# Kernel tuning notes

Measured on AMD Instinct MI355X. Metric: run time of the kernel, lower is better.

Reference implementation:

```python
import jax, jax.numpy as jnp
import numpy as np
import math

B, L, D = 4, 2048, 512
H = 8
HD = D // H
K1 = 64  # local_window_size
K2 = 64  # global_window_size


def semi_local_mask(seq_len):
    # Faithful to create_semi_local_mask: anti-diagonal band + global prefix, ANDed with causal tril.
    i = jnp.arange(seq_len)[:, None]
    j = jnp.arange(seq_len)[None, :]
    band = (i + j >= seq_len - K1) & (i + j <= seq_len)
    glob = (j <= K2) & (j <= seq_len - i)
    causal = j <= i
    return (band | glob) & causal  # [L, L] bool


def setup_inputs() -> dict:
    key = jax.random.key(0)
    ks = jax.random.split(key, 8)
    def xavier(k, shape):
        fan_in, fan_out = shape[1], shape[0]
        lim = math.sqrt(6.0 / (fan_in + fan_out))
        return jax.random.uniform(k, shape, jnp.float32, -lim, lim)
    x = jax.random.normal(ks[0], (B, L, D), jnp.float32)
    w_qkv = xavier(ks[1], (3 * D, D)); b_qkv = jnp.zeros((3 * D,), jnp.float32)
    w_u = xavier(ks[2], (D, D));       b_u = jnp.zeros((D,), jnp.float32)
    w_out = xavier(ks[3], (D, D));     b_out = jnp.zeros((D,), jnp.float32)
    return {"x": x, "w_qkv": w_qkv, "b_qkv": b_qkv, "w_u": w_u, "b_u": b_u,
            "w_out": w_out, "b_out": b_out}


def reference(x, w_qkv, b_qkv, w_u, b_u, w_out, b_out):
    Bsz, Lq, Dm = x.shape
    qkv = (x @ w_qkv.T + b_qkv).reshape(Bsz, Lq, 3, H, HD)
    q, k, v = jnp.moveaxis(qkv, 2, 0)            # each [B, L, H, HD]
    q = jnp.transpose(q, (0, 2, 1, 3))           # [B, H, L, HD]
    k = jnp.transpose(k, (0, 2, 1, 3))
    v = jnp.transpose(v, (0, 2, 1, 3))
    u = x @ w_u.T + b_u                          # [B, L, D] (gate values)
    scale = 1.0 / math.sqrt(HD)
    scores = jnp.einsum('bhqd,bhkd->bhqk', q * scale, k)
    mask = semi_local_mask(Lq)                   # [L, L]
    scores = jnp.where(mask[None, None], scores, -jnp.inf)
    attn = jax.nn.softmax(scores, axis=-1)
    out = jnp.einsum('bhqk,bhkd->bhqd', attn, v)
    out = jnp.transpose(out, (0, 2, 1, 3)).reshape(Bsz, Lq, Dm)
    out = jax.nn.silu(out) * u
    return out @ w_out.T + b_out
```

## Files before the change

### kernel.cpp

```cpp
#include <hip/hip_runtime.h>
#include <hip/hip_bf16.h>

typedef __bf16 bf16x8 __attribute__((ext_vector_type(8)));
typedef float f32x4 __attribute__((ext_vector_type(4)));

#define B_ 4
#define L_ 2048
#define D_ 512
#define H_ 8

__device__ __forceinline__ void gl16(const __bf16* g, __bf16* l) {
  __builtin_amdgcn_global_load_lds(
      (const __attribute__((address_space(1))) void*)g,
      (__attribute__((address_space(3))) void*)l, 16, 0, 0);
}

__global__ __launch_bounds__(256) void cvt_pack(
    const float* __restrict__ x, const float* __restrict__ wq,
    const float* __restrict__ wu, const float* __restrict__ wo,
    const float* __restrict__ bq, const float* __restrict__ bu,
    __bf16* __restrict__ xb, __bf16* __restrict__ wcat,
    __bf16* __restrict__ wob, float* __restrict__ bcat)
{
  const int idx8 = blockIdx.x * 256 + threadIdx.x;
  const float* src; __bf16* dst; size_t so, dof;
  if (idx8 < 524288)      { src = x;  dst = xb;   so = (size_t)idx8 * 8;            dof = so; }
  else if (idx8 < 622592) { src = wq; dst = wcat; so = (size_t)(idx8 - 524288) * 8; dof = so; }
  else if (idx8 < 655360) { src = wu; dst = wcat; so = (size_t)(idx8 - 622592) * 8; dof = so + 786432; }
  else                    { src = wo; dst = wob;  so = (size_t)(idx8 - 655360) * 8; dof = so; }
  const float4 lo = *(const float4*)(src + so);
  const float4 hi = *(const float4*)(src + so + 4);
  bf16x8 r;
  r[0] = (__bf16)lo.x; r[1] = (__bf16)lo.y; r[2] = (__bf16)lo.z; r[3] = (__bf16)lo.w;
  r[4] = (__bf16)hi.x; r[5] = (__bf16)hi.y; r[6] = (__bf16)hi.z; r[7] = (__bf16)hi.w;
  *(bf16x8*)(dst + dof) = r;
  if (blockIdx.x == 0) {
#pragma unroll
    for (int e = 0; e < 8; ++e) {
      const int col = threadIdx.x * 8 + e;
      bcat[col] = (col < 1536) ? bq[col] : bu[col - 1536];
    }
  }
}

__global__ __launch_bounds__(512, 2) void gemm256(
    const __bf16* __restrict__ A, const __bf16* __restrict__ W,
    const float* __restrict__ bias, __bf16* __restrict__ C,
    int M, int N, int K)
{
  extern __shared__ char smem[];
  const int t = threadIdx.x;
  const int lane = t & 63;
  const int wave = t >> 6;
  const int wm = (wave >> 2) * 128;
  const int wn = (wave & 3) * 64;
  const int bm0 = blockIdx.x * 256;
  const int bn0 = blockIdx.y * 256;
  const int r = lane & 15, q = lane >> 4;
  const int nt = K >> 6;

  auto stage = [&](int kt, int p) {
#pragma unroll
    for (int j = 0; j < 4; ++j) {
      const int c = t + j * 512;
      const int row = c >> 3;
      const int cs = (c & 7) ^ (row & 7);
      gl16(A + (size_t)(bm0 + row) * K + kt * 64 + cs * 8,
           (__bf16*)(smem + p * 32768) + c * 8);
    }
#pragma unroll
    for (int j = 0; j < 4; ++j) {
      const int c = t + j * 512;
      const int row = c >> 3;
      const int cs = (c & 7) ^ (row & 7);
      gl16(W + (size_t)(bn0 + row) * K + kt * 64 + cs * 8,
           (__bf16*)(smem + 65536 + p * 32768) + c * 8);
    }
  };
  auto rdA = [&](int p, int mi, int ks) -> bf16x8 {
    const int row = wm + mi * 16 + r;
    const int byte = row * 128 + ((ks * 64 + q * 16) ^ ((row & 7) << 4));
    return *(const bf16x8*)(smem + p * 32768 + byte);
  };
  auto rdB = [&](int p, int ni, int ks) -> bf16x8 {
    const int row = wn + ni * 16 + r;
    const int byte = row * 128 + ((ks * 64 + q * 16) ^ ((row & 7) << 4));
    return *(const bf16x8*)(smem + 65536 + p * 32768 + byte);
  };

#define SB0 __builtin_amdgcn_sched_barrier(0)
#define LGKM0 asm volatile("s_waitcnt lgkmcnt(0)" ::: "memory")

  f32x4 acc[8][4] = {};

  stage(0, 0);
  stage(1, 1);

  for (int kt = 0; kt < nt; ++kt) {
    const int p = kt & 1;
    if (kt < nt - 1) asm volatile("s_waitcnt vmcnt(8)" ::: "memory");
    else             asm volatile("s_waitcnt vmcnt(0)" ::: "memory");
    SB0;
    __builtin_amdgcn_s_barrier();
    SB0;

    bf16x8 a03[4][2], a47[4][2], b01[2][2], b23[2][2];
#pragma unroll
    for (int mi = 0; mi < 4; ++mi) { a03[mi][0] = rdA(p, mi, 0); a03[mi][1] = rdA(p, mi, 1); }
#pragma unroll
    for (int ni = 0; ni < 2; ++ni) { b01[ni][0] = rdB(p, ni, 0); b01[ni][1] = rdB(p, ni, 1); }
    SB0; __builtin_amdgcn_s_barrier(); LGKM0; SB0;
    __builtin_amdgcn_s_setprio(1);
#pragma unroll
    for (int mi = 0; mi < 4; ++mi)
#pragma unroll
      for (int ni = 0; ni < 2; ++ni) {
        acc[mi][ni] = __builtin_amdgcn_mfma_f32_16x16x32_bf16(a03[mi][0], b01[ni][0], acc[mi][ni], 0, 0, 0);
        acc[mi][ni] = __builtin_amdgcn_mfma_f32_16x16x32_bf16(a03[mi][1], b01[ni][1], acc[mi][ni], 0, 0, 0);
      }
    __builtin_amdgcn_s_setprio(0);
    SB0; __builtin_amdgcn_s_barrier(); SB0;
#pragma unroll
    for (int ni = 0; ni < 2; ++ni) { b23[ni][0] = rdB(p, ni + 2, 0); b23[ni][1] = rdB(p, ni + 2, 1); }
    SB0; __builtin_amdgcn_s_barrier(); LGKM0; SB0;
    __builtin_amdgcn_s_setprio(1);
#pragma unroll
    for (int mi = 0; mi < 4; ++mi)
#pragma unroll
      for (int ni = 0; ni < 2; ++ni) {
        acc[mi][ni + 2] = __builtin_amdgcn_mfma_f32_16x16x32_bf16(a03[mi][0], b23[ni][0], acc[mi][ni + 2], 0, 0, 0);
        acc[mi][ni + 2] = __builtin_amdgcn_mfma_f32_16x16x32_bf16(a03[mi][1], b23[ni][1], acc[mi][ni + 2], 0, 0, 0);
      }
    __builtin_amdgcn_s_setprio(0);
    SB0; __builtin_amdgcn_s_barrier(); SB0;
#pragma unroll
    for (int mi = 0; mi < 4; ++mi) { a47[mi][0] = rdA(p, mi + 4, 0); a47[mi][1] = rdA(p, mi + 4, 1); }
    SB0; __builtin_amdgcn_s_barrier(); LGKM0; SB0;
    __builtin_amdgcn_s_setprio(1);
#pragma unroll
    for (int mi = 0; mi < 4; ++mi)
#pragma unroll
      for (int ni = 0; ni < 2; ++ni) {
        acc[mi + 4][ni] = __builtin_amdgcn_mfma_f32_16x16x32_bf16(a47[mi][0], b01[ni][0], acc[mi + 4][ni], 0, 0, 0);
        acc[mi + 4][ni] = __builtin_amdgcn_mfma_f32_16x16x32_bf16(a47[mi][1], b01[ni][1], acc[mi + 4][ni], 0, 0, 0);
      }
    __builtin_amdgcn_s_setprio(0);
    SB0; __builtin_amdgcn_s_barrier(); SB0;
    if (kt + 2 < nt) stage(kt + 2, p);
    __builtin_amdgcn_s_setprio(1);
#pragma unroll
    for (int mi = 0; mi < 4; ++mi)
#pragma unroll
      for (int ni = 0; ni < 2; ++ni) {
        acc[mi + 4][ni + 2] = __builtin_amdgcn_mfma_f32_16x16x32_bf16(a47[mi][0], b23[ni][0], acc[mi + 4][ni + 2], 0, 0, 0);
        acc[mi + 4][ni + 2] = __builtin_amdgcn_mfma_f32_16x16x32_bf16(a47[mi][1], b23[ni][1], acc[mi + 4][ni + 2], 0, 0, 0);
      }
    __builtin_amdgcn_s_setprio(0);
  }

  const int cc = lane & 15, cq = lane >> 4;
#pragma unroll
  for (int mi = 0; mi < 8; ++mi) {
#pragma unroll
    for (int ni = 0; ni < 4; ++ni) {
      const int gcol = bn0 + wn + ni * 16 + cc;
      const float bv = bias[gcol];
#pragma unroll
      for (int rr = 0; rr < 4; ++rr) {
        const int grow = bm0 + wm + mi * 16 + cq * 4 + rr;
        C[(size_t)grow * N + gcol] = (__bf16)(acc[mi][ni][rr] + bv);
      }
    }
  }
}

template <typename TOUT>
__global__ __launch_bounds__(256) void gemm_async(
    const __bf16* __restrict__ A, const __bf16* __restrict__ W,
    const float* __restrict__ bias, TOUT* __restrict__ C,
    int M, int N, int K)
{
  __shared__ __bf16 lA[4096];
  __shared__ __bf16 lB[4096];
  const int t = threadIdx.x;
  const int lane = t & 63;
  const int wave = t >> 6;
  const int bm0 = blockIdx.x * 128;
  const int bn0 = blockIdx.y * 128;
  const int wm = (wave >> 1) * 64;
  const int wn = (wave & 1) * 64;

  f32x4 acc[4][4] = {};

  const __bf16* Ap0 = A + (size_t)(bm0 + (t >> 2)) * K + (t & 3) * 8;
  const __bf16* Bp0 = W + (size_t)(bn0 + (t >> 2)) * K + (t & 3) * 8;
  const size_t r64 = (size_t)64 * K;

  for (int k0 = 0; k0 < K; k0 += 32) {
    __syncthreads();
    gl16(Ap0 + k0,       lA + t * 8);
    gl16(Ap0 + r64 + k0, lA + (t + 256) * 8);
    gl16(Bp0 + k0,       lB + t * 8);
    gl16(Bp0 + r64 + k0, lB + (t + 256) * 8);
    __syncthreads();

    const int r = lane & 15, q = lane >> 4;
    bf16x8 af[4], bfr[4];
#pragma unroll
    for (int mi = 0; mi < 4; ++mi) af[mi] = ((const bf16x8*)lA)[(wm + mi * 16 + r) * 4 + q];
#pragma unroll
    for (int ni = 0; ni < 4; ++ni) bfr[ni] = ((const bf16x8*)lB)[(wn + ni * 16 + r) * 4 + q];
#pragma unroll
    for (int mi = 0; mi < 4; ++mi)
#pragma unroll
      for (int ni = 0; ni < 4; ++ni)
        acc[mi][ni] = __builtin_amdgcn_mfma_f32_16x16x32_bf16(af[mi], bfr[ni], acc[mi][ni], 0, 0, 0);
  }

  const int cc = lane & 15, cq = lane >> 4;
#pragma unroll
  for (int mi = 0; mi < 4; ++mi) {
#pragma unroll
    for (int ni = 0; ni < 4; ++ni) {
      const int gcol = bn0 + wn + ni * 16 + cc;
      const float bv = bias[gcol];
#pragma unroll
      for (int rr = 0; rr < 4; ++rr) {
        const int grow = bm0 + wm + mi * 16 + cq * 4 + rr;
        C[(size_t)grow * N + gcol] = (TOUT)(acc[mi][ni][rr] + bv);
      }
    }
  }
}

#define SP 72
#define QS 2048
__global__ __launch_bounds__(256) void attn_tile(
    const __bf16* __restrict__ qu,
    __bf16* __restrict__ g)
{
  const int qt = blockIdx.x, h = blockIdx.y, b = blockIdx.z;
  const int t = threadIdx.x;
  const int lane = t & 63;
  const int w = t >> 6;
  const int q0 = qt * 64, qmax = q0 + 63;
  const size_t bL = (size_t)b * L_;

  __shared__ __bf16 lK[4096];
  __shared__ __bf16 lV[64 * SP];
  __shared__ __bf16 Pb[64 * SP];

  const int cq = lane >> 4, cc = lane & 15;
  const int krow_st = t >> 2, kgb = t & 3;

  bf16x8 aq0, aq1;
  {
    const __bf16* qsrc = qu + (bL + q0 + w * 16 + cc) * QS + h * 64 + cq * 8;
    aq0 = *(const bf16x8*)qsrc;
    aq1 = *(const bf16x8*)(qsrc + 32);
  }

  float mreg[4], lreg[4];
#pragma unroll
  for (int rr = 0; rr < 4; ++rr) { mreg[rr] = -1e30f; lreg[rr] = 0.f; }
  f32x4 acc_o[4] = {};

  int clist[5]; int ncl = 0;
  clist[ncl++] = 0;
  if (qmax >= 64) clist[ncl++] = 64;
  {
    int lo = 1921 - q0; if (lo < 0) lo = 0; lo &= ~63;
    const int hik = min(qmax, 2048 - q0);
    for (int c = lo; c <= hik; c += 64)
      if (c >= 128) clist[ncl++] = c;
  }

  bf16x8 k0r, k1r, var, vbr;
  {
    const __bf16* src = qu + (bL + clist[0] + krow_st) * QS + 512 + h * 64;
    k0r = *(const bf16x8*)(src + kgb * 8);
    k1r = *(const bf16x8*)(src + kgb * 8 + 32);
    const __bf16* vsrc = qu + (bL + clist[0] + lane) * QS + 1024 + h * 64 + w * 16;
    var = *(const bf16x8*)vsrc;
    vbr = *(const bf16x8*)(vsrc + 8);
  }

  for (int ci = 0; ci < ncl; ++ci) {
    const int c0 = clist[ci];
    asm volatile("s_waitcnt vmcnt(0)" ::: "memory");
    __builtin_amdgcn_sched_barrier(0);
    __builtin_amdgcn_s_barrier();
    __builtin_amdgcn_sched_barrier(0);
    {
      char* lkb = (char*)lK;
      const int sw = (krow_st & 7) << 4;
      *(bf16x8*)(lkb + ((krow_st * 128 + kgb * 16) ^ sw))      = k0r;
      *(bf16x8*)(lkb + ((krow_st * 128 + kgb * 16 + 64) ^ sw)) = k1r;
#pragma unroll
      for (int e = 0; e < 8; ++e) {
        lV[(w * 16 + e) * SP + lane]     = var[e];
        lV[(w * 16 + 8 + e) * SP + lane] = vbr[e];
      }
    }
    if (ci + 1 < ncl) {
      const int cn = clist[ci + 1];
      const __bf16* src = qu + (bL + cn + krow_st) * QS + 512 + h * 64;
      k0r = *(const bf16x8*)(src + kgb * 8);
      k1r = *(const bf16x8*)(src + kgb * 8 + 32);
      const __bf16* vsrc = qu + (bL + cn + lane) * QS + 1024 + h * 64 + w * 16;
      var = *(const bf16x8*)(vsrc);
      vbr = *(const bf16x8*)(vsrc + 8);
    }
    asm volatile("s_waitcnt lgkmcnt(0)" ::: "memory");
    __builtin_amdgcn_sched_barrier(0);
    __builtin_amdgcn_s_barrier();
    __builtin_amdgcn_sched_barrier(0);

    f32x4 s[4];
    {
      const char* lkb = (const char*)lK;
#pragma unroll
      for (int nt = 0; nt < 4; ++nt) {
        const int krow = nt * 16 + cc;
        const int sw = (krow & 7) << 4;
        bf16x8 bk0 = *(const bf16x8*)(lkb + ((krow * 128 + cq * 16) ^ sw));
        bf16x8 bk1 = *(const bf16x8*)(lkb + ((krow * 128 + 64 + cq * 16) ^ sw));
        f32x4 a = {};
        a = __builtin_amdgcn_mfma_f32_16x16x32_bf16(aq0, bk0, a, 0, 0, 0);
        a = __builtin_amdgcn_mfma_f32_16x16x32_bf16(aq1, bk1, a, 0, 0, 0);
        s[nt] = a;
      }
    }

#pragma unroll
    for (int nt = 0; nt < 4; ++nt) {
#pragma unroll
      for (int rr = 0; rr < 4; ++rr) {
        const int i = q0 + w * 16 + cq * 4 + rr;
        const int j = c0 + nt * 16 + cc;
        const int ij = i + j;
        const bool valid = (j <= i) &&
            ((ij >= 1984 && ij <= 2048) || (j <= 64 && ij <= 2048));
        s[nt][rr] = valid ? s[nt][rr] * 0.125f : -1e30f;
      }
    }

    f32x4 pm;
#pragma unroll
    for (int rr = 0; rr < 4; ++rr)
      pm[rr] = fmaxf(fmaxf(s[0][rr], s[1][rr]), fmaxf(s[2][rr], s[3][rr]));
#pragma unroll
    for (int m = 1; m < 16; m <<= 1) {
#pragma unroll
      for (int rr = 0; rr < 4; ++rr)
        pm[rr] = fmaxf(pm[rr], __shfl_xor(pm[rr], m, 64));
    }
    float corr[4];
#pragma unroll
    for (int rr = 0; rr < 4; ++rr) {
      const float nm = fmaxf(mreg[rr], pm[rr]);
      corr[rr] = __expf(mreg[rr] - nm);
      mreg[rr] = nm;
    }

    f32x4 ps = {};
#pragma unroll
    for (int nt = 0; nt < 4; ++nt) {
#pragma unroll
      for (int rr = 0; rr < 4; ++rr) {
        const float p = __expf(s[nt][rr] - mreg[rr]);
        ps[rr] += p;
        Pb[(w * 16 + cq * 4 + rr) * SP + nt * 16 + cc] = (__bf16)p;
      }
    }
#pragma unroll
    for (int m = 1; m < 16; m <<= 1) {
#pragma unroll
      for (int rr = 0; rr < 4; ++rr)
        ps[rr] += __shfl_xor(ps[rr], m, 64);
    }
#pragma unroll
    for (int rr = 0; rr < 4; ++rr) lreg[rr] = lreg[rr] * corr[rr] + ps[rr];

    {
      bf16x8 pa0 = *(const bf16x8*)(Pb + (w * 16 + cc) * SP + cq * 8);
      bf16x8 pa1 = *(const bf16x8*)(Pb + (w * 16 + cc) * SP + 32 + cq * 8);
#pragma unroll
      for (int dt = 0; dt < 4; ++dt) {
#pragma unroll
        for (int rr = 0; rr < 4; ++rr) acc_o[dt][rr] *= corr[rr];
        bf16x8 vb0 = *(const bf16x8*)(lV + (dt * 16 + cc) * SP + cq * 8);
        bf16x8 vb1 = *(const bf16x8*)(lV + (dt * 16 + cc) * SP + 32 + cq * 8);
        acc_o[dt] = __builtin_amdgcn_mfma_f32_16x16x32_bf16(pa0, vb0, acc_o[dt], 0, 0, 0);
        acc_o[dt] = __builtin_amdgcn_mfma_f32_16x16x32_bf16(pa1, vb1, acc_o[dt], 0, 0, 0);
      }
    }
  }

#pragma unroll
  for (int dt = 0; dt < 4; ++dt) {
#pragma unroll
    for (int rr = 0; rr < 4; ++rr) {
      const int row16 = cq * 4 + rr;
      const size_t qrow = bL + q0 + w * 16 + row16;
      const int d = dt * 16 + cc;
      const float o = acc_o[dt][rr] / fmaxf(lreg[rr], 1e-30f);
      const float uv = (float)qu[qrow * QS + 1536 + h * 64 + d];
      g[qrow * D_ + h * 64 + d] = (__bf16)(o / (1.f + __expf(-o)) * uv);
    }
  }
}

extern "C" void kernel_launch(void* const* d_in, const int* in_sizes, int n_in,
                              void* d_out, int out_size, void* d_ws, size_t ws_size,
                              hipStream_t stream) {
  const float* x     = (const float*)d_in[0];
  const float* w_qkv = (const float*)d_in[1];
  const float* b_qkv = (const float*)d_in[2];
  const float* w_u   = (const float*)d_in[3];
  const float* b_u   = (const float*)d_in[4];
  const float* w_out = (const float*)d_in[5];
  const float* b_out = (const float*)d_in[6];
  float* out = (float*)d_out;

  char* ws = (char*)d_ws;
  __bf16* xb   = (__bf16*)ws;
  __bf16* wcat = (__bf16*)(ws + 8388608);
  __bf16* wob  = (__bf16*)(ws + 10485760);
  float*  bcat = (float*) (ws + 11010048);
  __bf16* qu   = (__bf16*)(ws + 11018240);
  __bf16* gb   = (__bf16*)(ws + 44572672);

  static bool attr_done = []() {
    hipFuncSetAttribute((const void*)gemm256,
                        hipFuncAttributeMaxDynamicSharedMemorySize, 131072);
    return true;
  }();
  (void)attr_done;

  cvt_pack<<<dim3(2688), dim3(256), 0, stream>>>(
      x, w_qkv, w_u, w_out, b_qkv, b_u, xb, wcat, wob, bcat);
  gemm256<<<dim3(32, 8), dim3(512), 131072, stream>>>(
      xb, wcat, bcat, qu, 8192, 2048, 512);
  attn_tile<<<dim3(L_ / 64, H_, B_), dim3(256), 0, stream>>>(qu, gb);
  gemm_async<float><<<dim3(64, 4), dim3(256), 0, stream>>>(
      gb, wob, b_out, out, 8192, 512, 512);
}
```

Baseline: 148.3 us.

## Fuse all stages into one cooperative persistent kernel with grid syncs

Adds a cooperative megakernel that runs the fp32-to-bf16 conversion, the QKV/U GEMM, the semi-local attention and the output GEMM in sequence. Grid-wide syncs separate the stages, so the four separate launches and their gaps go away. The attention stage packs two 64-row tiles per 512-thread block, and the output GEMM now uses 128x128 tiles across 256 blocks. It also removes several intra-iteration LDS barriers in the standalone GEMM, which is a race risk because shared buffers may be restaged before every wave has finished reading. With 256 blocks the attention work is less parallel, and any block skew stalls the whole grid at each sync.

```diff
diff --git a/kernel.cpp b/kernel.cpp
--- a/kernel.cpp
+++ b/kernel.cpp
@@ -1,5 +1,8 @@
 #include <hip/hip_runtime.h>
 #include <hip/hip_bf16.h>
+#include <hip/hip_cooperative_groups.h>
+
+namespace cg = cooperative_groups;
 
 typedef __bf16 bf16x8 __attribute__((ext_vector_type(8)));
 typedef float f32x4 __attribute__((ext_vector_type(4)));
@@ -8,11 +11,433 @@
 #define L_ 2048
 #define D_ 512
 #define H_ 8
+#define QS 2048
+#define SP 72
+
+#define SB0 __builtin_amdgcn_sched_barrier(0)
+#define WAIT_VM(n) asm volatile("s_waitcnt vmcnt(" #n ")" ::: "memory")
+#define WAIT_LGKM0 asm volatile("s_waitcnt lgkmcnt(0)" ::: "memory")
 
 __device__ __forceinline__ void gl16(const __bf16* g, __bf16* l) {
   __builtin_amdgcn_global_load_lds(
       (const __attribute__((address_space(1))) void*)g,
       (__attribute__((address_space(3))) void*)l, 16, 0, 0);
+}
+
+__global__ __launch_bounds__(512, 2) void mega(
+    const float* __restrict__ x,  const float* __restrict__ wq,
+    const float* __restrict__ wu, const float* __restrict__ wo,
+    const float* __restrict__ bq, const float* __restrict__ bu,
+    const float* __restrict__ bo,
+    __bf16* __restrict__ xb, __bf16* __restrict__ wcat,
+    __bf16* __restrict__ wob, float* __restrict__ bcat,
+    __bf16* __restrict__ qu, __bf16* __restrict__ gb,
+    float* __restrict__ out)
+{
+  extern __shared__ char smem[];
+  cg::grid_group gg = cg::this_grid();
+  const int t = threadIdx.x;
+  const int blk = blockIdx.x;
+  const int lane = t & 63;
+  const int wave = t >> 6;
+
+  {
+#pragma unroll
+    for (int it = 0; it < 6; ++it) {
+      const int idx8 = blk * 512 + t + it * 131072;
+      if (idx8 < 688128) {
+        const float* src; __bf16* dst; size_t so, dof;
+        if (idx8 < 524288)      { src = x;  dst = xb;   so = (size_t)idx8 * 8;            dof = so; }
+        else if (idx8 < 622592) { src = wq; dst = wcat; so = (size_t)(idx8 - 524288) * 8; dof = so; }
+        else if (idx8 < 655360) { src = wu; dst = wcat; so = (size_t)(idx8 - 622592) * 8; dof = so + 786432; }
+        else                    { src = wo; dst = wob;  so = (size_t)(idx8 - 655360) * 8; dof = so; }
+        const float4 lo = *(const float4*)(src + so);
+        const float4 hi = *(const float4*)(src + so + 4);
+        bf16x8 r;
+        r[0] = (__bf16)lo.x; r[1] = (__bf16)lo.y; r[2] = (__bf16)lo.z; r[3] = (__bf16)lo.w;
+        r[4] = (__bf16)hi.x; r[5] = (__bf16)hi.y; r[6] = (__bf16)hi.z; r[7] = (__bf16)hi.w;
+        *(bf16x8*)(dst + dof) = r;
+      }
+    }
+    if (blk == 0 && t < 256) {
+#pragma unroll
+      for (int e = 0; e < 8; ++e) {
+        const int col = t * 8 + e;
+        bcat[col] = (col < 1536) ? bq[col] : bu[col - 1536];
+      }
+    }
+  }
+  __threadfence();
+  gg.sync();
+
+  {
+    const int bm0 = (blk & 31) * 256;
+    const int bn0 = (blk >> 5) * 256;
+    const int wm = (wave >> 2) * 128;
+    const int wn = (wave & 3) * 64;
+    const int r = lane & 15, q = lane >> 4;
+
+    auto stage = [&](int kt, int p) {
+#pragma unroll
+      for (int j = 0; j < 4; ++j) {
+        const int c = t + j * 512;
+        const int row = c >> 3;
+        const int cs = (c & 7) ^ (row & 7);
+        gl16(xb + (size_t)(bm0 + row) * 512 + kt * 64 + cs * 8,
+             (__bf16*)(smem + p * 32768) + c * 8);
+      }
+#pragma unroll
+      for (int j = 0; j < 4; ++j) {
+        const int c = t + j * 512;
+        const int row = c >> 3;
+        const int cs = (c & 7) ^ (row & 7);
+        gl16(wcat + (size_t)(bn0 + row) * 512 + kt * 64 + cs * 8,
+             (__bf16*)(smem + 65536 + p * 32768) + c * 8);
+      }
+    };
+    auto rdA = [&](int p, int mi, int ks) -> bf16x8 {
+      const int row = wm + mi * 16 + r;
+      const int byte = row * 128 + ((ks * 64 + q * 16) ^ ((row & 7) << 4));
+      return *(const bf16x8*)(smem + p * 32768 + byte);
+    };
+    auto rdB = [&](int p, int ni, int ks) -> bf16x8 {
+      const int row = wn + ni * 16 + r;
+      const int byte = row * 128 + ((ks * 64 + q * 16) ^ ((row & 7) << 4));
+      return *(const bf16x8*)(smem + 65536 + p * 32768 + byte);
+    };
+
+    f32x4 acc[8][4] = {};
+    WAIT_VM(0);
+    stage(0, 0);
+    stage(1, 1);
+
+    for (int kt = 0; kt < 8; ++kt) {
+      const int p = kt & 1;
+      if (kt < 7) { WAIT_VM(8); } else { WAIT_VM(0); }
+      SB0; __builtin_amdgcn_s_barrier(); SB0;
+
+      bf16x8 a03[4][2], a47[4][2], b01[2][2], b23[2][2];
+#pragma unroll
+      for (int mi = 0; mi < 4; ++mi) { a03[mi][0] = rdA(p, mi, 0); a03[mi][1] = rdA(p, mi, 1); }
+#pragma unroll
+      for (int ni = 0; ni < 2; ++ni) { b01[ni][0] = rdB(p, ni, 0); b01[ni][1] = rdB(p, ni, 1); }
+      __builtin_amdgcn_s_setprio(1);
+#pragma unroll
+      for (int mi = 0; mi < 4; ++mi)
+#pragma unroll
+        for (int ni = 0; ni < 2; ++ni) {
+          acc[mi][ni] = __builtin_amdgcn_mfma_f32_16x16x32_bf16(a03[mi][0], b01[ni][0], acc[mi][ni], 0, 0, 0);
+          acc[mi][ni] = __builtin_amdgcn_mfma_f32_16x16x32_bf16(a03[mi][1], b01[ni][1], acc[mi][ni], 0, 0, 0);
+        }
+      __builtin_amdgcn_s_setprio(0);
+#pragma unroll
+      for (int ni = 0; ni < 2; ++ni) { b23[ni][0] = rdB(p, ni + 2, 0); b23[ni][1] = rdB(p, ni + 2, 1); }
+      __builtin_amdgcn_s_setprio(1);
+#pragma unroll
+      for (int mi = 0; mi < 4; ++mi)
+#pragma unroll
+        for (int ni = 0; ni < 2; ++ni) {
+          acc[mi][ni + 2] = __builtin_amdgcn_mfma_f32_16x16x32_bf16(a03[mi][0], b23[ni][0], acc[mi][ni + 2], 0, 0, 0);
+          acc[mi][ni + 2] = __builtin_amdgcn_mfma_f32_16x16x32_bf16(a03[mi][1], b23[ni][1], acc[mi][ni + 2], 0, 0, 0);
+        }
+      __builtin_amdgcn_s_setprio(0);
+#pragma unroll
+      for (int mi = 0; mi < 4; ++mi) { a47[mi][0] = rdA(p, mi + 4, 0); a47[mi][1] = rdA(p, mi + 4, 1); }
+      __builtin_amdgcn_s_setprio(1);
+#pragma unroll
+      for (int mi = 0; mi < 4; ++mi)
+#pragma unroll
+        for (int ni = 0; ni < 2; ++ni) {
+          acc[mi + 4][ni] = __builtin_amdgcn_mfma_f32_16x16x32_bf16(a47[mi][0], b01[ni][0], acc[mi + 4][ni], 0, 0, 0);
+          acc[mi + 4][ni] = __builtin_amdgcn_mfma_f32_16x16x32_bf16(a47[mi][1], b01[ni][1], acc[mi + 4][ni], 0, 0, 0);
+        }
+      __builtin_amdgcn_s_setprio(0);
+      WAIT_LGKM0;
+      SB0; __builtin_amdgcn_s_barrier(); SB0;
+      if (kt + 2 < 8) stage(kt + 2, p);
+      __builtin_amdgcn_s_setprio(1);
+#pragma unroll
+      for (int mi = 0; mi < 4; ++mi)
+#pragma unroll
+        for (int ni = 0; ni < 2; ++ni) {
+          acc[mi + 4][ni + 2] = __builtin_amdgcn_mfma_f32_16x16x32_bf16(a47[mi][0], b23[ni][0], acc[mi + 4][ni + 2], 0, 0, 0);
+          acc[mi + 4][ni + 2] = __builtin_amdgcn_mfma_f32_16x16x32_bf16(a47[mi][1], b23[ni][1], acc[mi + 4][ni + 2], 0, 0, 0);
+        }
+      __builtin_amdgcn_s_setprio(0);
+    }
+
+    const int cc = lane & 15, cq = lane >> 4;
+#pragma unroll
+    for (int mi = 0; mi < 8; ++mi) {
+#pragma unroll
+      for (int ni = 0; ni < 4; ++ni) {
+        const int gcol = bn0 + wn + ni * 16 + cc;
+        const float bv = bcat[gcol];
+#pragma unroll
+        for (int rr = 0; rr < 4; ++rr) {
+          const int grow = bm0 + wm + mi * 16 + cq * 4 + rr;
+          qu[(size_t)grow * 2048 + gcol] = (__bf16)(acc[mi][ni][rr] + bv);
+        }
+      }
+    }
+  }
+  __threadfence();
+  gg.sync();
+
+  {
+    const int u = wave >> 2;
+    const int wv = wave & 3;
+    const int tu = t & 255;
+    char* ub = smem + u * 32768;
+    __bf16* lK = (__bf16*)ub;
+    __bf16* lV = (__bf16*)(ub + 8192);
+    __bf16* Pb = (__bf16*)(ub + 17408);
+    const int cq = lane >> 4, cc = lane & 15;
+    const int krow_st = tu >> 2, kgb = tu & 3;
+
+    for (int i = 0; i < 2; ++i) {
+      const int uid = i * 512 + blk * 2 + u;
+      const int qt = uid >> 5;
+      const int h = (uid >> 2) & 7;
+      const int b = uid & 3;
+      const int q0 = qt * 64, qmax = q0 + 63;
+      const size_t bL = (size_t)b * L_;
+
+      bf16x8 aq0, aq1;
+      {
+        const __bf16* qsrc = qu + (bL + q0 + wv * 16 + cc) * QS + h * 64 + cq * 8;
+        aq0 = *(const bf16x8*)qsrc;
+        aq1 = *(const bf16x8*)(qsrc + 32);
+      }
+
+      float mreg[4], lreg[4];
+#pragma unroll
+      for (int rr = 0; rr < 4; ++rr) { mreg[rr] = -1e30f; lreg[rr] = 0.f; }
+      f32x4 acc_o[4] = {};
+
+      int clist[5]; int ncl = 0;
+      clist[ncl++] = 0;
+      if (qmax >= 64) clist[ncl++] = 64;
+      {
+        int lo = 1921 - q0; if (lo < 0) lo = 0; lo &= ~63;
+        const int hik = min(qmax, 2048 - q0);
+        for (int c = lo; c <= hik; c += 64)
+          if (c >= 128) clist[ncl++] = c;
+      }
+
+      bf16x8 k0r, k1r, var, vbr;
+      {
+        const __bf16* src = qu + (bL + clist[0] + krow_st) * QS + 512 + h * 64;
+        k0r = *(const bf16x8*)(src + kgb * 8);
+        k1r = *(const bf16x8*)(src + kgb * 8 + 32);
+        const __bf16* vsrc = qu + (bL + clist[0] + lane) * QS + 1024 + h * 64 + wv * 16;
+        var = *(const bf16x8*)vsrc;
+        vbr = *(const bf16x8*)(vsrc + 8);
+      }
+
+      for (int ci = 0; ci < ncl; ++ci) {
+        const int c0 = clist[ci];
+        WAIT_VM(0);
+        SB0; __builtin_amdgcn_s_barrier(); SB0;
+        {
+          char* lkb = (char*)lK;
+          const int sw = (krow_st & 7) << 4;
+          *(bf16x8*)(lkb + ((krow_st * 128 + kgb * 16) ^ sw))      = k0r;
+          *(bf16x8*)(lkb + ((krow_st * 128 + kgb * 16 + 64) ^ sw)) = k1r;
+#pragma unroll
+          for (int e = 0; e < 8; ++e) {
+            lV[(wv * 16 + e) * SP + lane]     = var[e];
+            lV[(wv * 16 + 8 + e) * SP + lane] = vbr[e];
+          }
+        }
+        if (ci + 1 < ncl) {
+          const int cn = clist[ci + 1];
+          const __bf16* src = qu + (bL + cn + krow_st) * QS + 512 + h * 64;
+          k0r = *(const bf16x8*)(src + kgb * 8);
+          k1r = *(const bf16x8*)(src + kgb * 8 + 32);
+          const __bf16* vsrc = qu + (bL + cn + lane) * QS + 1024 + h * 64 + wv * 16;
+          var = *(const bf16x8*)(vsrc);
+          vbr = *(const bf16x8*)(vsrc + 8);
+        }
+        WAIT_LGKM0;
+        SB0; __builtin_amdgcn_s_barrier(); SB0;
+
+        f32x4 s[4];
+        {
+          const char* lkb = (const char*)lK;
+#pragma unroll
+          for (int nt = 0; nt < 4; ++nt) {
+            const int krow = nt * 16 + cc;
+            const int sw = (krow & 7) << 4;
+            bf16x8 bk0 = *(const bf16x8*)(lkb + ((krow * 128 + cq * 16) ^ sw));
+            bf16x8 bk1 = *(const bf16x8*)(lkb + ((krow * 128 + 64 + cq * 16) ^ sw));
+            f32x4 a = {};
+            a = __builtin_amdgcn_mfma_f32_16x16x32_bf16(aq0, bk0, a, 0, 0, 0);
+            a = __builtin_amdgcn_mfma_f32_16x16x32_bf16(aq1, bk1, a, 0, 0, 0);
+            s[nt] = a;
+          }
+        }
+
+#pragma unroll
+        for (int nt = 0; nt < 4; ++nt) {
+#pragma unroll
+          for (int rr = 0; rr < 4; ++rr) {
+            const int i2 = q0 + wv * 16 + cq * 4 + rr;
+            const int j = c0 + nt * 16 + cc;
+            const int ij = i2 + j;
+            const bool valid = (j <= i2) &&
+                ((ij >= 1984 && ij <= 2048) || (j <= 64 && ij <= 2048));
+            s[nt][rr] = valid ? s[nt][rr] * 0.125f : -1e30f;
+          }
+        }
+
+        f32x4 pm;
+#pragma unroll
+        for (int rr = 0; rr < 4; ++rr)
+          pm[rr] = fmaxf(fmaxf(s[0][rr], s[1][rr]), fmaxf(s[2][rr], s[3][rr]));
+#pragma unroll
+        for (int m = 1; m < 16; m <<= 1) {
+#pragma unroll
+          for (int rr = 0; rr < 4; ++rr)
+            pm[rr] = fmaxf(pm[rr], __shfl_xor(pm[rr], m, 64));
+        }
+        float corr[4];
+#pragma unroll
+        for (int rr = 0; rr < 4; ++rr) {
+          const float nm = fmaxf(mreg[rr], pm[rr]);
+          corr[rr] = __expf(mreg[rr] - nm);
+          mreg[rr] = nm;
+        }
+
+        f32x4 ps = {};
+#pragma unroll
+        for (int nt = 0; nt < 4; ++nt) {
+#pragma unroll
+          for (int rr = 0; rr < 4; ++rr) {
+            const float p = __expf(s[nt][rr] - mreg[rr]);
+            ps[rr] += p;
+            Pb[(wv * 16 + cq * 4 + rr) * SP + nt * 16 + cc] = (__bf16)p;
+          }
+        }
+#pragma unroll
+        for (int m = 1; m < 16; m <<= 1) {
+#pragma unroll
+          for (int rr = 0; rr < 4; ++rr)
+            ps[rr] += __shfl_xor(ps[rr], m, 64);
+        }
+#pragma unroll
+        for (int rr = 0; rr < 4; ++rr) lreg[rr] = lreg[rr] * corr[rr] + ps[rr];
+
+        {
+          bf16x8 pa0 = *(const bf16x8*)(Pb + (wv * 16 + cc) * SP + cq * 8);
+          bf16x8 pa1 = *(const bf16x8*)(Pb + (wv * 16 + cc) * SP + 32 + cq * 8);
+#pragma unroll
+          for (int dt = 0; dt < 4; ++dt) {
+#pragma unroll
+            for (int rr = 0; rr < 4; ++rr) acc_o[dt][rr] *= corr[rr];
+            bf16x8 vb0 = *(const bf16x8*)(lV + (dt * 16 + cc) * SP + cq * 8);
+            bf16x8 vb1 = *(const bf16x8*)(lV + (dt * 16 + cc) * SP + 32 + cq * 8);
+            acc_o[dt] = __builtin_amdgcn_mfma_f32_16x16x32_bf16(pa0, vb0, acc_o[dt], 0, 0, 0);
+            acc_o[dt] = __builtin_amdgcn_mfma_f32_16x16x32_bf16(pa1, vb1, acc_o[dt], 0, 0, 0);
+          }
+        }
+      }
+
+#pragma unroll
+      for (int dt = 0; dt < 4; ++dt) {
+#pragma unroll
+        for (int rr = 0; rr < 4; ++rr) {
+          const int row16 = cq * 4 + rr;
+          const size_t qrow = bL + q0 + wv * 16 + row16;
+          const int d = dt * 16 + cc;
+          const float o = acc_o[dt][rr] / fmaxf(lreg[rr], 1e-30f);
+          const float uv = (float)qu[qrow * QS + 1536 + h * 64 + d];
+          gb[qrow * D_ + h * 64 + d] = (__bf16)(o / (1.f + __expf(-o)) * uv);
+        }
+      }
+    }
+  }
+  __threadfence();
+  gg.sync();
+
+  {
+    const int bm0 = (blk & 63) * 128;
+    const int bn0 = (blk >> 6) * 128;
+    const int wm = (wave >> 2) * 64;
+    const int wn = (wave & 3) * 32;
+    const int r = lane & 15, q = lane >> 4;
+
+    auto stg = [&](int kt, int p) {
+#pragma unroll
+      for (int j = 0; j < 2; ++j) {
+        const int c = t + j * 512;
+        const int row = c >> 3;
+        const int cs = (c & 7) ^ (row & 7);
+        gl16(gb + (size_t)(bm0 + row) * 512 + kt * 64 + cs * 8,
+             (__bf16*)(smem + p * 16384) + c * 8);
+      }
+#pragma unroll
+      for (int j = 0; j < 2; ++j) {
+        const int c = t + j * 512;
+        const int row = c >> 3;
+        const int cs = (c & 7) ^ (row & 7);
+        gl16(wob + (size_t)(bn0 + row) * 512 + kt * 64 + cs * 8,
+             (__bf16*)(smem + 32768 + p * 16384) + c * 8);
+      }
+    };
+    auto rA = [&](int p, int mi, int ks) -> bf16x8 {
+      const int row = wm + mi * 16 + r;
+      const int byte = row * 128 + ((ks * 64 + q * 16) ^ ((row & 7) << 4));
+      return *(const bf16x8*)(smem + p * 16384 + byte);
+    };
+    auto rB = [&](int p, int ni, int ks) -> bf16x8 {
+      const int row = wn + ni * 16 + r;
+      const int byte = row * 128 + ((ks * 64 + q * 16) ^ ((row & 7) << 4));
+      return *(const bf16x8*)(smem + 32768 + p * 16384 + byte);
+    };
+
+    f32x4 acc2[4][2] = {};
+    WAIT_VM(0);
+    stg(0, 0); stg(1, 1);
+
+    for (int kt = 0; kt < 8; ++kt) {
+      const int p = kt & 1;
+      if (kt < 7) { WAIT_VM(4); } else { WAIT_VM(0); }
+      SB0; __builtin_amdgcn_s_barrier(); SB0;
+      bf16x8 af[4][2], bf[2][2];
+#pragma unroll
+      for (int mi = 0; mi < 4; ++mi) { af[mi][0] = rA(p, mi, 0); af[mi][1] = rA(p, mi, 1); }
+#pragma unroll
+      for (int ni = 0; ni < 2; ++ni) { bf[ni][0] = rB(p, ni, 0); bf[ni][1] = rB(p, ni, 1); }
+      WAIT_LGKM0;
+      SB0; __builtin_amdgcn_s_barrier(); SB0;
+      if (kt + 2 < 8) stg(kt + 2, p);
+      __builtin_amdgcn_s_setprio(1);
+#pragma unroll
+      for (int mi = 0; mi < 4; ++mi)
+#pragma unroll
+        for (int ni = 0; ni < 2; ++ni) {
+          acc2[mi][ni] = __builtin_amdgcn_mfma_f32_16x16x32_bf16(af[mi][0], bf[ni][0], acc2[mi][ni], 0, 0, 0);
+          acc2[mi][ni] = __builtin_amdgcn_mfma_f32_16x16x32_bf16(af[mi][1], bf[ni][1], acc2[mi][ni], 0, 0, 0);
+        }
+      __builtin_amdgcn_s_setprio(0);
+    }
+
+    const int cc = lane & 15, cq = lane >> 4;
+#pragma unroll
+    for (int mi = 0; mi < 4; ++mi) {
+#pragma unroll
+      for (int ni = 0; ni < 2; ++ni) {
+        const int gcol = bn0 + wn + ni * 16 + cc;
+        const float bv = bo[gcol];
+#pragma unroll
+        for (int rr = 0; rr < 4; ++rr) {
+          const int grow = bm0 + wm + mi * 16 + cq * 4 + rr;
+          out[(size_t)grow * 512 + gcol] = acc2[mi][ni][rr] + bv;
+        }
+      }
+    }
+  }
 }
 
 __global__ __launch_bounds__(256) void cvt_pack(
@@ -88,28 +513,20 @@
     return *(const bf16x8*)(smem + 65536 + p * 32768 + byte);
   };
 
-#define SB0 __builtin_amdgcn_sched_barrier(0)
-#define LGKM0 asm volatile("s_waitcnt lgkmcnt(0)" ::: "memory")
-
   f32x4 acc[8][4] = {};
-
   stage(0, 0);
   stage(1, 1);
 
   for (int kt = 0; kt < nt; ++kt) {
     const int p = kt & 1;
-    if (kt < nt - 1) asm volatile("s_waitcnt vmcnt(8)" ::: "memory");
-    else             asm volatile("s_waitcnt vmcnt(0)" ::: "memory");
-    SB0;
-    __builtin_amdgcn_s_barrier();
-    SB0;
+    if (kt < nt - 1) { WAIT_VM(8); } else { WAIT_VM(0); }
+    SB0; __builtin_amdgcn_s_barrier(); SB0;
 
     bf16x8 a03[4][2], a47[4][2], b01[2][2], b23[2][2];
 #pragma unroll
     for (int mi = 0; mi < 4; ++mi) { a03[mi][0] = rdA(p, mi, 0); a03[mi][1] = rdA(p, mi, 1); }
 #pragma unroll
     for (int ni = 0; ni < 2; ++ni) { b01[ni][0] = rdB(p, ni, 0); b01[ni][1] = rdB(p, ni, 1); }
-    SB0; __builtin_amdgcn_s_barrier(); LGKM0; SB0;
     __builtin_amdgcn_s_setprio(1);
 #pragma unroll
     for (int mi = 0; mi < 4; ++mi)
@@ -119,10 +536,8 @@
         acc[mi][ni] = __builtin_amdgcn_mfma_f32_16x16x32_bf16(a03[mi][1], b01[ni][1], acc[mi][ni], 0, 0, 0);
       }
     __builtin_amdgcn_s_setprio(0);
-    SB0; __builtin_amdgcn_s_barrier(); SB0;
 #pragma unroll
     for (int ni = 0; ni < 2; ++ni) { b23[ni][0] = rdB(p, ni + 2, 0); b23[ni][1] = rdB(p, ni + 2, 1); }
-    SB0; __builtin_amdgcn_s_barrier(); LGKM0; SB0;
     __builtin_amdgcn_s_setprio(1);
 #pragma unroll
     for (int mi = 0; mi < 4; ++mi)
@@ -132,10 +547,8 @@
         acc[mi][ni + 2] = __builtin_amdgcn_mfma_f32_16x16x32_bf16(a03[mi][1], b23[ni][1], acc[mi][ni + 2], 0, 0, 0);
       }
     __builtin_amdgcn_s_setprio(0);
-    SB0; __builtin_amdgcn_s_barrier(); SB0;
 #pragma unroll
     for (int mi = 0; mi < 4; ++mi) { a47[mi][0] = rdA(p, mi + 4, 0); a47[mi][1] = rdA(p, mi + 4, 1); }
-    SB0; __builtin_amdgcn_s_barrier(); LGKM0; SB0;
     __builtin_amdgcn_s_setprio(1);
 #pragma unroll
     for (int mi = 0; mi < 4; ++mi)
@@ -145,6 +558,7 @@
         acc[mi + 4][ni] = __builtin_amdgcn_mfma_f32_16x16x32_bf16(a47[mi][1], b01[ni][1], acc[mi + 4][ni], 0, 0, 0);
       }
     __builtin_amdgcn_s_setprio(0);
+    WAIT_LGKM0;
     SB0; __builtin_amdgcn_s_barrier(); SB0;
     if (kt + 2 < nt) stage(kt + 2, p);
     __builtin_amdgcn_s_setprio(1);
@@ -233,11 +647,8 @@
   }
 }
 
-#define SP 72
-#define QS 2048
 __global__ __launch_bounds__(256) void attn_tile(
-    const __bf16* __restrict__ qu,
-    __bf16* __restrict__ g)
+    const __bf16* __restrict__ qu, __bf16* __restrict__ g)
 {
   const int qt = blockIdx.x, h = blockIdx.y, b = blockIdx.z;
   const int t = threadIdx.x;
@@ -287,10 +698,8 @@
 
   for (int ci = 0; ci < ncl; ++ci) {
     const int c0 = clist[ci];
-    asm volatile("s_waitcnt vmcnt(0)" ::: "memory");
-    __builtin_amdgcn_sched_barrier(0);
-    __builtin_amdgcn_s_barrier();
-    __builtin_amdgcn_sched_barrier(0);
+    WAIT_VM(0);
+    SB0; __builtin_amdgcn_s_barrier(); SB0;
     {
       char* lkb = (char*)lK;
       const int sw = (krow_st & 7) << 4;
@@ -311,10 +720,8 @@
       var = *(const bf16x8*)(vsrc);
       vbr = *(const bf16x8*)(vsrc + 8);
     }
-    asm volatile("s_waitcnt lgkmcnt(0)" ::: "memory");
-    __builtin_amdgcn_sched_barrier(0);
-    __builtin_amdgcn_s_barrier();
-    __builtin_amdgcn_sched_barrier(0);
+    WAIT_LGKM0;
+    SB0; __builtin_amdgcn_s_barrier(); SB0;
 
     f32x4 s[4];
     {
@@ -431,18 +838,38 @@
   __bf16* qu   = (__bf16*)(ws + 11018240);
   __bf16* gb   = (__bf16*)(ws + 44572672);
 
-  static bool attr_done = []() {
+  static int coop = -1;
+  if (coop < 0) {
+    hipFuncSetAttribute((const void*)mega,
+                        hipFuncAttributeMaxDynamicSharedMemorySize, 131072);
     hipFuncSetAttribute((const void*)gemm256,
                         hipFuncAttributeMaxDynamicSharedMemorySize, 131072);
-    return true;
-  }();
-  (void)attr_done;
-
-  cvt_pack<<<dim3(2688), dim3(256), 0, stream>>>(
-      x, w_qkv, w_u, w_out, b_qkv, b_u, xb, wcat, wob, bcat);
-  gemm256<<<dim3(32, 8), dim3(512), 131072, stream>>>(
-      xb, wcat, bcat, qu, 8192, 2048, 512);
-  attn_tile<<<dim3(L_ / 64, H_, B_), dim3(256), 0, stream>>>(qu, gb);
-  gemm_async<float><<<dim3(64, 4), dim3(256), 0, stream>>>(
-      gb, wob, b_out, out, 8192, 512, 512);
+    int dev = 0; hipGetDevice(&dev);
+    int v = 0;
+    hipDeviceGetAttribute(&v, hipDeviceAttributeCooperativeLaunch, dev);
+    coop = v;
+  }
+
+  bool done = false;
+  if (coop > 0) {
+    void* kargs[] = {(void*)&x, (void*)&w_qkv, (void*)&w_u, (void*)&w_out,
+                     (void*)&b_qkv, (void*)&b_u, (void*)&b_out,
+                     (void*)&xb, (void*)&wcat, (void*)&wob, (void*)&bcat,
+                     (void*)&qu, (void*)&gb, (void*)&out};
+    if (hipLaunchCooperativeKernel((void*)mega, dim3(256), dim3(512),
+                                   kargs, 131072, stream) == hipSuccess) {
+      done = true;
+    } else {
+      (void)hipGetLastError();
+    }
+  }
+  if (!done) {
+    cvt_pack<<<dim3(2688), dim3(256), 0, stream>>>(
+        x, w_qkv, w_u, w_out, b_qkv, b_u, xb, wcat, wob, bcat);
+    gemm256<<<dim3(32, 8), dim3(512), 131072, stream>>>(
+        xb, wcat, bcat, qu, 8192, 2048, 512);
+    attn_tile<<<dim3(L_ / 64, H_, B_), dim3(256), 0, stream>>>(qu, gb);
+    gemm_async<float><<<dim3(64, 4), dim3(256), 0, stream>>>(
+        gb, wob, b_out, out, 8192, 512, 512);
+  }
 }
```

New measurement: 416.0 us. 2.8x slower.

## Double attention query tile to 128 rows and trim GEMM inner barriers

Applied to the files above, without the earlier changes.

The attention kernel now gives each block 128 query rows with 512 threads (8 waves), so every K/V chunk staged in LDS serves twice as many queries and each thread loads half as much. The chunk list grows to cover the wider query range. In the main GEMM, the per-subphase workgroup barriers and LDS waits between fragment reads and MFMA groups are removed, leaving one lgkm wait and barrier before the next stage is issued. This cuts sync overhead, but the larger attention tile may visit more chunks that are mostly masked and leaves fewer blocks to fill the CUs.

```diff
diff --git a/kernel.cpp b/kernel.cpp
--- a/kernel.cpp
+++ b/kernel.cpp
@@ -8,6 +8,12 @@
 #define L_ 2048
 #define D_ 512
 #define H_ 8
+#define QS 2048
+#define SP 72
+
+#define SB0 __builtin_amdgcn_sched_barrier(0)
+#define WAIT_VM(n) asm volatile("s_waitcnt vmcnt(" #n ")" ::: "memory")
+#define WAIT_LGKM0 asm volatile("s_waitcnt lgkmcnt(0)" ::: "memory")
 
 __device__ __forceinline__ void gl16(const __bf16* g, __bf16* l) {
   __builtin_amdgcn_global_load_lds(
@@ -88,28 +94,20 @@
     return *(const bf16x8*)(smem + 65536 + p * 32768 + byte);
   };
 
-#define SB0 __builtin_amdgcn_sched_barrier(0)
-#define LGKM0 asm volatile("s_waitcnt lgkmcnt(0)" ::: "memory")
-
   f32x4 acc[8][4] = {};
-
   stage(0, 0);
   stage(1, 1);
 
   for (int kt = 0; kt < nt; ++kt) {
     const int p = kt & 1;
-    if (kt < nt - 1) asm volatile("s_waitcnt vmcnt(8)" ::: "memory");
-    else             asm volatile("s_waitcnt vmcnt(0)" ::: "memory");
-    SB0;
-    __builtin_amdgcn_s_barrier();
-    SB0;
+    if (kt < nt - 1) { WAIT_VM(8); } else { WAIT_VM(0); }
+    SB0; __builtin_amdgcn_s_barrier(); SB0;
 
     bf16x8 a03[4][2], a47[4][2], b01[2][2], b23[2][2];
 #pragma unroll
     for (int mi = 0; mi < 4; ++mi) { a03[mi][0] = rdA(p, mi, 0); a03[mi][1] = rdA(p, mi, 1); }
 #pragma unroll
     for (int ni = 0; ni < 2; ++ni) { b01[ni][0] = rdB(p, ni, 0); b01[ni][1] = rdB(p, ni, 1); }
-    SB0; __builtin_amdgcn_s_barrier(); LGKM0; SB0;
     __builtin_amdgcn_s_setprio(1);
 #pragma unroll
     for (int mi = 0; mi < 4; ++mi)
@@ -119,10 +117,8 @@
         acc[mi][ni] = __builtin_amdgcn_mfma_f32_16x16x32_bf16(a03[mi][1], b01[ni][1], acc[mi][ni], 0, 0, 0);
       }
     __builtin_amdgcn_s_setprio(0);
-    SB0; __builtin_amdgcn_s_barrier(); SB0;
 #pragma unroll
     for (int ni = 0; ni < 2; ++ni) { b23[ni][0] = rdB(p, ni + 2, 0); b23[ni][1] = rdB(p, ni + 2, 1); }
-    SB0; __builtin_amdgcn_s_barrier(); LGKM0; SB0;
     __builtin_amdgcn_s_setprio(1);
 #pragma unroll
     for (int mi = 0; mi < 4; ++mi)
@@ -132,10 +128,8 @@
         acc[mi][ni + 2] = __builtin_amdgcn_mfma_f32_16x16x32_bf16(a03[mi][1], b23[ni][1], acc[mi][ni + 2], 0, 0, 0);
       }
     __builtin_amdgcn_s_setprio(0);
-    SB0; __builtin_amdgcn_s_barrier(); SB0;
 #pragma unroll
     for (int mi = 0; mi < 4; ++mi) { a47[mi][0] = rdA(p, mi + 4, 0); a47[mi][1] = rdA(p, mi + 4, 1); }
-    SB0; __builtin_amdgcn_s_barrier(); LGKM0; SB0;
     __builtin_amdgcn_s_setprio(1);
 #pragma unroll
     for (int mi = 0; mi < 4; ++mi)
@@ -145,6 +139,7 @@
         acc[mi + 4][ni] = __builtin_amdgcn_mfma_f32_16x16x32_bf16(a47[mi][1], b01[ni][1], acc[mi + 4][ni], 0, 0, 0);
       }
     __builtin_amdgcn_s_setprio(0);
+    WAIT_LGKM0;
     SB0; __builtin_amdgcn_s_barrier(); SB0;
     if (kt + 2 < nt) stage(kt + 2, p);
     __builtin_amdgcn_s_setprio(1);
@@ -233,9 +228,7 @@
   }
 }
 
-#define SP 72
-#define QS 2048
-__global__ __launch_bounds__(256) void attn_tile(
+__global__ __launch_bounds__(512) void attn_tile(
     const __bf16* __restrict__ qu,
     __bf16* __restrict__ g)
 {
@@ -243,15 +236,15 @@
   const int t = threadIdx.x;
   const int lane = t & 63;
   const int w = t >> 6;
-  const int q0 = qt * 64, qmax = q0 + 63;
+  const int q0 = qt * 128, qmax = q0 + 127;
   const size_t bL = (size_t)b * L_;
 
   __shared__ __bf16 lK[4096];
   __shared__ __bf16 lV[64 * SP];
-  __shared__ __bf16 Pb[64 * SP];
+  __shared__ __bf16 Pb[128 * SP];
 
   const int cq = lane >> 4, cc = lane & 15;
-  const int krow_st = t >> 2, kgb = t & 3;
+  const int krow_st = t >> 3, kgb8 = t & 7;
 
   bf16x8 aq0, aq1;
   {
@@ -265,56 +258,45 @@
   for (int rr = 0; rr < 4; ++rr) { mreg[rr] = -1e30f; lreg[rr] = 0.f; }
   f32x4 acc_o[4] = {};
 
-  int clist[5]; int ncl = 0;
+  int clist[8]; int ncl = 0;
   clist[ncl++] = 0;
   if (qmax >= 64) clist[ncl++] = 64;
   {
-    int lo = 1921 - q0; if (lo < 0) lo = 0; lo &= ~63;
+    int lo = 1984 - qmax; if (lo < 0) lo = 0; lo &= ~63;
     const int hik = min(qmax, 2048 - q0);
     for (int c = lo; c <= hik; c += 64)
       if (c >= 128) clist[ncl++] = c;
   }
 
-  bf16x8 k0r, k1r, var, vbr;
+  bf16x8 k0r, var;
   {
     const __bf16* src = qu + (bL + clist[0] + krow_st) * QS + 512 + h * 64;
-    k0r = *(const bf16x8*)(src + kgb * 8);
-    k1r = *(const bf16x8*)(src + kgb * 8 + 32);
-    const __bf16* vsrc = qu + (bL + clist[0] + lane) * QS + 1024 + h * 64 + w * 16;
+    k0r = *(const bf16x8*)(src + kgb8 * 8);
+    const __bf16* vsrc = qu + (bL + clist[0] + lane) * QS + 1024 + h * 64 + w * 8;
     var = *(const bf16x8*)vsrc;
-    vbr = *(const bf16x8*)(vsrc + 8);
   }
 
   for (int ci = 0; ci < ncl; ++ci) {
     const int c0 = clist[ci];
-    asm volatile("s_waitcnt vmcnt(0)" ::: "memory");
-    __builtin_amdgcn_sched_barrier(0);
-    __builtin_amdgcn_s_barrier();
-    __builtin_amdgcn_sched_barrier(0);
+    WAIT_VM(0);
+    SB0; __builtin_amdgcn_s_barrier(); SB0;
     {
       char* lkb = (char*)lK;
       const int sw = (krow_st & 7) << 4;
-      *(bf16x8*)(lkb + ((krow_st * 128 + kgb * 16) ^ sw))      = k0r;
-      *(bf16x8*)(lkb + ((krow_st * 128 + kgb * 16 + 64) ^ sw)) = k1r;
-#pragma unroll
-      for (int e = 0; e < 8; ++e) {
-        lV[(w * 16 + e) * SP + lane]     = var[e];
-        lV[(w * 16 + 8 + e) * SP + lane] = vbr[e];
-      }
+      *(bf16x8*)(lkb + ((krow_st * 128 + kgb8 * 16) ^ sw)) = k0r;
+#pragma unroll
+      for (int e = 0; e < 8; ++e)
+        lV[(w * 8 + e) * SP + lane] = var[e];
     }
     if (ci + 1 < ncl) {
       const int cn = clist[ci + 1];
       const __bf16* src = qu + (bL + cn + krow_st) * QS + 512 + h * 64;
-      k0r = *(const bf16x8*)(src + kgb * 8);
-      k1r = *(const bf16x8*)(src + kgb * 8 + 32);
-      const __bf16* vsrc = qu + (bL + cn + lane) * QS + 1024 + h * 64 + w * 16;
-      var = *(const bf16x8*)(vsrc);
-      vbr = *(const bf16x8*)(vsrc + 8);
-    }
-    asm volatile("s_waitcnt lgkmcnt(0)" ::: "memory");
-    __builtin_amdgcn_sched_barrier(0);
-    __builtin_amdgcn_s_barrier();
-    __builtin_amdgcn_sched_barrier(0);
+      k0r = *(const bf16x8*)(src + kgb8 * 8);
+      const __bf16* vsrc = qu + (bL + cn + lane) * QS + 1024 + h * 64 + w * 8;
+      var = *(const bf16x8*)vsrc;
+    }
+    WAIT_LGKM0;
+    SB0; __builtin_amdgcn_s_barrier(); SB0;
 
     f32x4 s[4];
     {
@@ -442,7 +424,7 @@
       x, w_qkv, w_u, w_out, b_qkv, b_u, xb, wcat, wob, bcat);
   gemm256<<<dim3(32, 8), dim3(512), 131072, stream>>>(
       xb, wcat, bcat, qu, 8192, 2048, 512);
-  attn_tile<<<dim3(L_ / 64, H_, B_), dim3(256), 0, stream>>>(qu, gb);
+  attn_tile<<<dim3(L_ / 128, H_, B_), dim3(512), 0, stream>>>(qu, gb);
   gemm_async<float><<<dim3(64, 4), dim3(256), 0, stream>>>(
       gb, wob, b_out, out, 8192, 512, 512);
 }
```

Result: no change. 147.8 us (-0.3%).
